# Kernel optimization log

Hardware: AMD Instinct MI355X
Metric: run time of the kernel (lower is better)

Reference implementation:

```python
import jax, jax.numpy as jnp
import numpy as np

E = 1024
H = 16
HD = E // H
FF = 4 * E
B, T = 2, 2048


def _linear_params(key, fan_in, fan_out):
    k1, k2 = jax.random.split(key)
    bound = 1.0 / np.sqrt(fan_in)
    W = jax.random.uniform(k1, (fan_out, fan_in), jnp.float32, -bound, bound)
    b = jax.random.uniform(k2, (fan_out,), jnp.float32, -bound, bound)
    return W, b


def setup_inputs() -> dict:
    key = jax.random.key(0)
    keys = jax.random.split(key, 8)
    x = jax.random.normal(keys[0], (B, T, E), jnp.float32)
    Wq, bq = _linear_params(keys[1], E, E)
    Wk, bk = _linear_params(keys[2], E, E)
    Wv, bv = _linear_params(keys[3], E, E)
    Wo, bo = _linear_params(keys[4], E, E)
    W1, b1 = _linear_params(keys[5], E, FF)
    W2, b2 = _linear_params(keys[6], FF, E)
    ln1_g = jnp.ones((E,), jnp.float32); ln1_b = jnp.zeros((E,), jnp.float32)
    ln2_g = jnp.ones((E,), jnp.float32); ln2_b = jnp.zeros((E,), jnp.float32)
    return {"x": x, "Wq": Wq, "bq": bq, "Wk": Wk, "bk": bk, "Wv": Wv, "bv": bv,
            "Wo": Wo, "bo": bo, "W1": W1, "b1": b1, "W2": W2, "b2": b2,
            "ln1_g": ln1_g, "ln1_b": ln1_b, "ln2_g": ln2_g, "ln2_b": ln2_b}


def _layernorm(x, g, b, eps=1e-5):
    mu = jnp.mean(x, axis=-1, keepdims=True)
    var = jnp.var(x, axis=-1, keepdims=True)
    return (x - mu) * jax.lax.rsqrt(var + eps) * g + b


def reference(x, Wq, bq, Wk, bk, Wv, bv, Wo, bo, W1, b1, W2, b2,
              ln1_g, ln1_b, ln2_g, ln2_b):
    Bc, Tc, Ec = x.shape
    h = _layernorm(x, ln1_g, ln1_b)
    # projections (torch Linear: y = x @ W.T + b)
    q = (h @ Wq.T + bq).reshape(Bc, Tc, H, HD).transpose(0, 2, 1, 3)  # [B,H,T,hd]
    k = (h @ Wk.T + bk).reshape(Bc, Tc, H, HD).transpose(0, 2, 1, 3)
    v = (h @ Wv.T + bv).reshape(Bc, Tc, H, HD).transpose(0, 2, 1, 3)
    scores = jnp.einsum('bhqd,bhkd->bhqk', q, k) / np.sqrt(HD).astype(np.float32)
    causal = jnp.tril(jnp.ones((Tc, Tc), bool))
    scores = jnp.where(causal, scores, -jnp.inf)
    att = jax.nn.softmax(scores, axis=-1)  # dropout = identity (eval)
    out = jnp.einsum('bhqk,bhkd->bhqd', att, v)
    out = out.transpose(0, 2, 1, 3).reshape(Bc, Tc, Ec)
    x = x + out @ Wo.T + bo
    h2 = _layernorm(x, ln2_g, ln2_b)
    ff = jax.nn.relu(h2 @ W1.T + b1) @ W2.T + b2
    return x + ff
```

## Files before the change

### kernel.cpp

```cpp
#include <hip/hip_runtime.h>

typedef unsigned short u16;
typedef __bf16 bf16x8 __attribute__((ext_vector_type(8)));
typedef float f32x4 __attribute__((ext_vector_type(4)));

#define E_ 1024
#define T_ 2048
#define B_ 2
#define H_ 16
#define FF_ 4096
#define M_ 4096

__device__ __forceinline__ u16 f2b(float f) {
    union { float f; unsigned u; } c; c.f = f;
    unsigned r = c.u + 0x7FFFu + ((c.u >> 16) & 1u);
    return (u16)(r >> 16);
}
__device__ __forceinline__ u16 f2bt(float f) {
    union { float f; unsigned u; } c; c.f = f;
    return (u16)(c.u >> 16);
}

__device__ __forceinline__ void gl16(const u16* g, u16* l) {
    __builtin_amdgcn_global_load_lds(
        (__attribute__((address_space(1))) void*)g,
        (__attribute__((address_space(3))) void*)l, 16, 0, 0);
}

__global__ __launch_bounds__(256) void cvt_ln(
        const float* __restrict__ Wq, const float* __restrict__ Wk,
        const float* __restrict__ Wv, const float* __restrict__ Wo,
        const float* __restrict__ W1, const float* __restrict__ W2,
        const float* __restrict__ bq, const float* __restrict__ bk,
        const float* __restrict__ bv,
        u16* __restrict__ WqkvB, u16* __restrict__ WoB,
        u16* __restrict__ W1B, u16* __restrict__ W2B,
        float* __restrict__ bqkv,
        const float* __restrict__ x, const float* __restrict__ g1,
        const float* __restrict__ b1v, u16* __restrict__ hB) {
    if (blockIdx.x < 1024) {
        int row = blockIdx.x * 4 + (threadIdx.x >> 6);
        int t = threadIdx.x & 63;
        const float* xr = x + (size_t)row * E_;
        float v[16];
        float sum = 0.f, ss = 0.f;
#pragma unroll
        for (int c = 0; c < 4; c++) {
            float4 f = *(const float4*)&xr[c * 256 + t * 4];
            v[c * 4 + 0] = f.x; v[c * 4 + 1] = f.y; v[c * 4 + 2] = f.z; v[c * 4 + 3] = f.w;
            sum += f.x + f.y + f.z + f.w;
            ss += f.x * f.x + f.y * f.y + f.z * f.z + f.w * f.w;
        }
#pragma unroll
        for (int d = 32; d; d >>= 1) {
            sum += __shfl_xor(sum, d);
            ss  += __shfl_xor(ss, d);
        }
        float mu = sum * (1.f / E_);
        float var = ss * (1.f / E_) - mu * mu;
        float rs = rsqrtf(var + 1e-5f);
#pragma unroll
        for (int c = 0; c < 4; c++) {
            int idx = c * 256 + t * 4;
            float4 g4 = *(const float4*)&g1[idx];
            float4 b4 = *(const float4*)&b1v[idx];
            ushort4 o;
            o.x = f2b((v[c * 4 + 0] - mu) * rs * g4.x + b4.x);
            o.y = f2b((v[c * 4 + 1] - mu) * rs * g4.y + b4.y);
            o.z = f2b((v[c * 4 + 2] - mu) * rs * g4.z + b4.z);
            o.w = f2b((v[c * 4 + 3] - mu) * rs * g4.w + b4.w);
            *(ushort4*)&hB[(size_t)row * E_ + idx] = o;
        }
        return;
    }
    int i = (blockIdx.x - 1024) * 256 + threadIdx.x;
    if (i >= 3146496) return;
    if (i >= 3145728) {
        int j = i - 3145728;
        const float* s = (j < 256) ? bq : (j < 512) ? bk : bv;
        int jj = j & 255;
        *(float4*)&bqkv[j * 4] = *(const float4*)&s[jj * 4];
        return;
    }
    const float* src; u16* dst; int j;
    if (i < 786432) {
        src = (i < 262144) ? Wq : (i < 524288) ? Wk : Wv;
        j = i & 262143;
        dst = WqkvB + (i >> 18) * (E_ * E_);
    } else if (i < 1048576) { j = i - 786432;  src = Wo; dst = WoB; }
    else if (i < 2097152)   { j = i - 1048576; src = W1; dst = W1B; }
    else                    { j = i - 2097152; src = W2; dst = W2B; }
    float4 f = *(const float4*)&src[j * 4];
    ushort4 o;
    o.x = f2b(f.x); o.y = f2b(f.y); o.z = f2b(f.z); o.w = f2b(f.w);
    *(ushort4*)&dst[j * 4] = o;
}

__global__ __launch_bounds__(64) void ln_fwd(u16* __restrict__ out, const float* __restrict__ x,
                                             const float* __restrict__ g, const float* __restrict__ bta) {
    int row = blockIdx.x;
    int t = threadIdx.x;
    const float* xr = x + (size_t)row * E_;
    float v[16];
    float sum = 0.f, ss = 0.f;
#pragma unroll
    for (int c = 0; c < 4; c++) {
        float4 f = *(const float4*)&xr[c * 256 + t * 4];
        v[c * 4 + 0] = f.x; v[c * 4 + 1] = f.y; v[c * 4 + 2] = f.z; v[c * 4 + 3] = f.w;
        sum += f.x + f.y + f.z + f.w;
        ss += f.x * f.x + f.y * f.y + f.z * f.z + f.w * f.w;
    }
#pragma unroll
    for (int d = 32; d; d >>= 1) {
        sum += __shfl_xor(sum, d);
        ss  += __shfl_xor(ss, d);
    }
    float mu = sum * (1.f / E_);
    float var = ss * (1.f / E_) - mu * mu;
    float rs = rsqrtf(var + 1e-5f);
#pragma unroll
    for (int c = 0; c < 4; c++) {
        int idx = c * 256 + t * 4;
        float4 g4 = *(const float4*)&g[idx];
        float4 b4 = *(const float4*)&bta[idx];
        ushort4 o;
        o.x = f2b((v[c * 4 + 0] - mu) * rs * g4.x + b4.x);
        o.y = f2b((v[c * 4 + 1] - mu) * rs * g4.y + b4.y);
        o.z = f2b((v[c * 4 + 2] - mu) * rs * g4.z + b4.z);
        o.w = f2b((v[c * 4 + 3] - mu) * rs * g4.w + b4.w);
        *(ushort4*)&out[(size_t)row * E_ + idx] = o;
    }
}

template<int BM>
__global__ __launch_bounds__(256) void gemm_bt(
        const u16* __restrict__ A, const u16* __restrict__ Bt,
        const float* __restrict__ bias, const float* __restrict__ residual,
        float* __restrict__ outF, u16* __restrict__ outB, u16* __restrict__ outVt,
        int M, int N, int K, int relu, int qkvmode) {
    constexpr int MT = BM / 32;
    __shared__ __align__(16) u16 As[2][BM * 32];
    __shared__ __align__(16) u16 Bs[2][128 * 32];
    int tid = threadIdx.x;
    int m0 = blockIdx.y * BM, n0 = blockIdx.x * 128;
    int wave = tid >> 6, lane = tid & 63;
    int wm = wave & 1, wn = wave >> 1;
    int r16 = lane & 15, kg = lane >> 4;

    const u16* gA = A + (size_t)(m0 + wave * (BM / 4) + (lane >> 2)) * K + (lane & 3) * 8;
    const u16* gB = Bt + (size_t)(n0 + wave * 32 + (lane >> 2)) * K + (lane & 3) * 8;
    size_t row16 = (size_t)16 * K;
    int aoff = wave * (BM / 4) * 32;
    int boff = wave * 1024;

    f32x4 acc[MT][4] = {};

    const int nk = K >> 5;
    gl16(gA, As[0] + aoff);
    if (BM == 128) gl16(gA + row16, As[0] + aoff + 512);
    gl16(gB, Bs[0] + boff);
    gl16(gB + row16, Bs[0] + boff + 512);

    for (int ks = 0; ks < nk; ks++) {
        int cur = ks & 1;
        __syncthreads();
        if (ks + 1 < nk) {
            int k1 = (ks + 1) << 5;
            int nxt = cur ^ 1;
            gl16(gA + k1, As[nxt] + aoff);
            if (BM == 128) gl16(gA + k1 + row16, As[nxt] + aoff + 512);
            gl16(gB + k1, Bs[nxt] + boff);
            gl16(gB + k1 + row16, Bs[nxt] + boff + 512);
        }

        bf16x8 af[MT], bfr[4];
#pragma unroll
        for (int mt = 0; mt < MT; mt++)
            af[mt] = *(const bf16x8*)&As[cur][(wm * (BM / 2) + mt * 16 + r16) * 32 + kg * 8];
#pragma unroll
        for (int nt = 0; nt < 4; nt++)
            bfr[nt] = *(const bf16x8*)&Bs[cur][(wn * 64 + nt * 16 + r16) * 32 + kg * 8];
#pragma unroll
        for (int mt = 0; mt < MT; mt++)
#pragma unroll
            for (int nt = 0; nt < 4; nt++)
                acc[mt][nt] = __builtin_amdgcn_mfma_f32_16x16x32_bf16(af[mt], bfr[nt], acc[mt][nt], 0, 0, 0);
    }

#pragma unroll
    for (int mt = 0; mt < MT; mt++) {
#pragma unroll
        for (int nt = 0; nt < 4; nt++) {
            int gm = m0 + wm * (BM / 2) + mt * 16 + kg * 4;
            int gn = n0 + wn * 64 + nt * 16 + r16;
            float bv = bias[gn];
            if (qkvmode) {
                if (gn < 2048) {
                    float scl = (gn < 1024) ? 0.18033688f : 1.0f;
#pragma unroll
                    for (int r = 0; r < 4; r++)
                        outB[(size_t)(gm + r) * 2048 + gn] = f2b((acc[mt][nt][r] + bv) * scl);
                } else {
                    int bq_ = gm >> 11, tq = gm & 2047, d = gn - 2048;
                    ushort4 ov;
                    ov.x = f2b(acc[mt][nt][0] + bv);
                    ov.y = f2b(acc[mt][nt][1] + bv);
                    ov.z = f2b(acc[mt][nt][2] + bv);
                    ov.w = f2b(acc[mt][nt][3] + bv);
                    *(ushort4*)&outVt[((size_t)(bq_ * 1024 + d)) * 2048 + tq] = ov;
                }
            } else {
#pragma unroll
                for (int r = 0; r < 4; r++) {
                    float v = acc[mt][nt][r] + bv;
                    size_t off = (size_t)(gm + r) * N + gn;
                    if (residual) v += residual[off];
                    if (relu) v = fmaxf(v, 0.f);
                    if (outF) outF[off] = v;
                    else outB[off] = f2b(v);
                }
            }
        }
    }
}

#define AST 68
__global__ __launch_bounds__(256) void attn_mfma(
        const u16* __restrict__ qk, const u16* __restrict__ vt,
        u16* __restrict__ out) {
    __shared__ __align__(16) u16 Ks[2][64 * AST];
    __shared__ __align__(16) u16 Vs[2][64 * AST];
    __shared__ __align__(16) u16 Ps[4][16 * AST];

    int bz = blockIdx.x;
    int h  = bz & 15;
    int b  = (bz >> 4) & 1;
    int qt = bz >> 5;

    int tid = threadIdx.x;
    int w = tid >> 6, lane = tid & 63;
    int g = lane >> 4, l16 = lane & 15;

    int qrow = qt * 64 + w * 16 + l16;
    bf16x8 qf[2];
    qf[0] = *(const bf16x8*)&qk[(size_t)(b * T_ + qrow) * 2048 + h * 64 + g * 8];
    qf[1] = *(const bf16x8*)&qk[(size_t)(b * T_ + qrow) * 2048 + h * 64 + 32 + g * 8];

    f32x4 o[4] = {};
    f32x4 lp = {0.f, 0.f, 0.f, 0.f};

    int r1 = tid >> 3, col1 = (tid & 7) * 8;
    const u16* gK = qk + (size_t)(b * T_) * 2048 + 1024 + h * 64;
    const u16* gV = vt + (size_t)(b * 1024 + h * 64) * 2048;

    uint4 kr1 = *(const uint4*)&gK[(size_t)r1 * 2048 + col1];
    uint4 kr2 = *(const uint4*)&gK[(size_t)(r1 + 32) * 2048 + col1];
    uint4 vr1 = *(const uint4*)&gV[(size_t)r1 * 2048 + col1];
    uint4 vr2 = *(const uint4*)&gV[(size_t)(r1 + 32) * 2048 + col1];

    for (int t = 0; t <= qt; t++) {
        int cur = t & 1;
        *(uint4*)&Ks[cur][r1 * AST + col1] = kr1;
        *(uint4*)&Ks[cur][(r1 + 32) * AST + col1] = kr2;
        *(uint4*)&Vs[cur][r1 * AST + col1] = vr1;
        *(uint4*)&Vs[cur][(r1 + 32) * AST + col1] = vr2;
        __syncthreads();
        if (t < qt) {
            int j1 = (t + 1) * 64;
            kr1 = *(const uint4*)&gK[(size_t)(j1 + r1) * 2048 + col1];
            kr2 = *(const uint4*)&gK[(size_t)(j1 + r1 + 32) * 2048 + col1];
            vr1 = *(const uint4*)&gV[(size_t)r1 * 2048 + j1 + col1];
            vr2 = *(const uint4*)&gV[(size_t)(r1 + 32) * 2048 + j1 + col1];
        }

        f32x4 s[4];
#pragma unroll
        for (int nt = 0; nt < 4; nt++) {
            f32x4 c16 = {-16.f, -16.f, -16.f, -16.f};
            bf16x8 k0 = *(const bf16x8*)&Ks[cur][(nt * 16 + l16) * AST + g * 8];
            bf16x8 k1 = *(const bf16x8*)&Ks[cur][(nt * 16 + l16) * AST + 32 + g * 8];
            s[nt] = __builtin_amdgcn_mfma_f32_16x16x32_bf16(qf[0], k0, c16, 0, 0, 0);
            s[nt] = __builtin_amdgcn_mfma_f32_16x16x32_bf16(qf[1], k1, s[nt], 0, 0, 0);
        }

        if (t == qt) {
            int j0 = t * 64;
#pragma unroll
            for (int nt = 0; nt < 4; nt++) {
                int key = j0 + nt * 16 + l16;
#pragma unroll
                for (int r = 0; r < 4; r++) {
                    int q = qt * 64 + w * 16 + g * 4 + r;
                    if (key > q) s[nt][r] = -INFINITY;
                }
            }
        }

#pragma unroll
        for (int nt = 0; nt < 4; nt++)
#pragma unroll
            for (int r = 0; r < 4; r++) {
                float p = exp2f(s[nt][r]);
                lp[r] += p;
                Ps[w][(g * 4 + r) * AST + nt * 16 + l16] = f2bt(p);
            }

#pragma unroll
        for (int kf = 0; kf < 2; kf++) {
            bf16x8 pf = *(const bf16x8*)&Ps[w][l16 * AST + kf * 32 + g * 8];
#pragma unroll
            for (int nt = 0; nt < 4; nt++) {
                bf16x8 vf = *(const bf16x8*)&Vs[cur][(nt * 16 + l16) * AST + kf * 32 + g * 8];
                o[nt] = __builtin_amdgcn_mfma_f32_16x16x32_bf16(pf, vf, o[nt], 0, 0, 0);
            }
        }
    }

#pragma unroll
    for (int x = 1; x <= 8; x <<= 1)
#pragma unroll
        for (int r = 0; r < 4; r++)
            lp[r] += __shfl_xor(lp[r], x);

    float inv[4];
#pragma unroll
    for (int r = 0; r < 4; r++) inv[r] = 1.f / lp[r];
    int qg = qt * 64 + w * 16 + g * 4;
#pragma unroll
    for (int nt = 0; nt < 4; nt++)
#pragma unroll
        for (int r = 0; r < 4; r++)
            out[(size_t)(b * T_ + qg + r) * E_ + h * 64 + nt * 16 + l16] =
                f2b(o[nt][r] * inv[r]);
}

extern "C" void kernel_launch(void* const* d_in, const int* in_sizes, int n_in,
                              void* d_out, int out_size, void* d_ws, size_t ws_size,
                              hipStream_t stream) {
    const float* x    = (const float*)d_in[0];
    const float* Wq   = (const float*)d_in[1];
    const float* bq   = (const float*)d_in[2];
    const float* Wk   = (const float*)d_in[3];
    const float* bk   = (const float*)d_in[4];
    const float* Wv   = (const float*)d_in[5];
    const float* bv   = (const float*)d_in[6];
    const float* Wo   = (const float*)d_in[7];
    const float* bo   = (const float*)d_in[8];
    const float* W1   = (const float*)d_in[9];
    const float* b1   = (const float*)d_in[10];
    const float* W2   = (const float*)d_in[11];
    const float* b2   = (const float*)d_in[12];
    const float* ln1g = (const float*)d_in[13];
    const float* ln1b = (const float*)d_in[14];
    const float* ln2g = (const float*)d_in[15];
    const float* ln2b = (const float*)d_in[16];

    char* ws = (char*)d_ws;
    size_t off = 0;
    auto alloc = [&](size_t bytes) { char* p = ws + off; off += (bytes + 255) & ~(size_t)255; return p; };

    u16*   hB    = (u16*)  alloc((size_t)M_ * E_ * 2);
    u16*   WqkvB = (u16*)  alloc((size_t)3 * E_ * E_ * 2);
    u16*   WoB   = (u16*)  alloc((size_t)E_ * E_ * 2);
    u16*   W1B   = (u16*)  alloc((size_t)FF_ * E_ * 2);
    u16*   W2B   = (u16*)  alloc((size_t)E_ * FF_ * 2);
    float* bqkv  = (float*)alloc(3 * E_ * 4);
    u16*   qkB   = (u16*)  alloc((size_t)M_ * 2 * E_ * 2);
    u16*   vtG   = (u16*)  alloc((size_t)M_ * E_ * 2);
    u16*   attnB = (u16*)  alloc((size_t)M_ * E_ * 2);
    float* x2    = (float*)alloc((size_t)M_ * E_ * 4);
    u16*   h2B   = (u16*)  alloc((size_t)M_ * E_ * 2);
    u16*   rB    = (u16*)  alloc((size_t)M_ * FF_ * 2);

    cvt_ln<<<1024 + 12291, 256, 0, stream>>>(Wq, Wk, Wv, Wo, W1, W2, bq, bk, bv,
                                             WqkvB, WoB, W1B, W2B, bqkv,
                                             x, ln1g, ln1b, hB);

    gemm_bt<128><<<dim3(3 * E_ / 128, M_ / 128), 256, 0, stream>>>(
        hB, WqkvB, bqkv, nullptr, nullptr, qkB, vtG, M_, 3 * E_, E_, 0, 1);

    attn_mfma<<<B_ * H_ * (T_ / 64), 256, 0, stream>>>(qkB, vtG, attnB);

    gemm_bt<64><<<dim3(E_ / 128, M_ / 64), 256, 0, stream>>>(
        attnB, WoB, bo, x, x2, nullptr, nullptr, M_, E_, E_, 0, 0);

    ln_fwd<<<M_, 64, 0, stream>>>(h2B, x2, ln2g, ln2b);

    gemm_bt<128><<<dim3(FF_ / 128, M_ / 128), 256, 0, stream>>>(
        h2B, W1B, b1, nullptr, nullptr, rB, nullptr, M_, FF_, E_, 1, 0);

    gemm_bt<64><<<dim3(E_ / 128, M_ / 64), 256, 0, stream>>>(
        rB, W2B, b2, x2, (float*)d_out, nullptr, nullptr, M_, E_, FF_, 0, 0);
}
```

Baseline: 392.0 us.

## Triple-buffer GEMM LDS tiles with explicit vmcnt waits; larger tile for FFN down-proj

The GEMM main loop moves from double to triple buffering. It prefetches two k-steps ahead and uses s_waitcnt vmcnt with a single barrier per iteration instead of a full drain before each step, so global-to-LDS loads overlap more with the MFMA work. The W2 down-projection also switches from 64-row to 128-row tiles, which halves its grid to 256 blocks. The changes use more LDS per block and cut parallelism for that GEMM, and correctness depends on the vmcnt counts matching the number of loads issued.

```diff
diff --git a/kernel.cpp b/kernel.cpp
--- a/kernel.cpp
+++ b/kernel.cpp
@@ -139,8 +139,8 @@
         float* __restrict__ outF, u16* __restrict__ outB, u16* __restrict__ outVt,
         int M, int N, int K, int relu, int qkvmode) {
     constexpr int MT = BM / 32;
-    __shared__ __align__(16) u16 As[2][BM * 32];
-    __shared__ __align__(16) u16 Bs[2][128 * 32];
+    __shared__ __align__(16) u16 As[3][BM * 32];
+    __shared__ __align__(16) u16 Bs[3][128 * 32];
     int tid = threadIdx.x;
     int m0 = blockIdx.y * BM, n0 = blockIdx.x * 128;
     int wave = tid >> 6, lane = tid & 63;
@@ -156,36 +156,50 @@
     f32x4 acc[MT][4] = {};
 
     const int nk = K >> 5;
-    gl16(gA, As[0] + aoff);
-    if (BM == 128) gl16(gA + row16, As[0] + aoff + 512);
-    gl16(gB, Bs[0] + boff);
-    gl16(gB + row16, Bs[0] + boff + 512);
-
-    for (int ks = 0; ks < nk; ks++) {
-        int cur = ks & 1;
-        __syncthreads();
-        if (ks + 1 < nk) {
-            int k1 = (ks + 1) << 5;
-            int nxt = cur ^ 1;
-            gl16(gA + k1, As[nxt] + aoff);
-            if (BM == 128) gl16(gA + k1 + row16, As[nxt] + aoff + 512);
-            gl16(gB + k1, Bs[nxt] + boff);
-            gl16(gB + k1 + row16, Bs[nxt] + boff + 512);
-        }
-
+
+    auto issue = [&](int kt, int buf) {
+        int k1 = kt << 5;
+        gl16(gA + k1, As[buf] + aoff);
+        if (BM == 128) gl16(gA + k1 + row16, As[buf] + aoff + 512);
+        gl16(gB + k1, Bs[buf] + boff);
+        gl16(gB + k1 + row16, Bs[buf] + boff + 512);
+    };
+
+    auto compute = [&](int cb) {
         bf16x8 af[MT], bfr[4];
 #pragma unroll
         for (int mt = 0; mt < MT; mt++)
-            af[mt] = *(const bf16x8*)&As[cur][(wm * (BM / 2) + mt * 16 + r16) * 32 + kg * 8];
+            af[mt] = *(const bf16x8*)&As[cb][(wm * (BM / 2) + mt * 16 + r16) * 32 + kg * 8];
 #pragma unroll
         for (int nt = 0; nt < 4; nt++)
-            bfr[nt] = *(const bf16x8*)&Bs[cur][(wn * 64 + nt * 16 + r16) * 32 + kg * 8];
+            bfr[nt] = *(const bf16x8*)&Bs[cb][(wn * 64 + nt * 16 + r16) * 32 + kg * 8];
 #pragma unroll
         for (int mt = 0; mt < MT; mt++)
 #pragma unroll
             for (int nt = 0; nt < 4; nt++)
                 acc[mt][nt] = __builtin_amdgcn_mfma_f32_16x16x32_bf16(af[mt], bfr[nt], acc[mt][nt], 0, 0, 0);
-    }
+    };
+
+    issue(0, 0);
+    issue(1, 1);
+
+    int cur = 0;
+    for (int ks = 0; ks < nk - 1; ks++) {
+        if (BM == 128) asm volatile("s_waitcnt vmcnt(4)" ::: "memory");
+        else           asm volatile("s_waitcnt vmcnt(3)" ::: "memory");
+        __builtin_amdgcn_s_barrier();
+        asm volatile("" ::: "memory");
+        if (ks + 2 < nk) {
+            int p2 = cur ? cur - 1 : 2;
+            issue(ks + 2, p2);
+        }
+        compute(cur);
+        cur = (cur < 2) ? cur + 1 : 0;
+    }
+    asm volatile("s_waitcnt vmcnt(0)" ::: "memory");
+    __builtin_amdgcn_s_barrier();
+    asm volatile("" ::: "memory");
+    compute(cur);
 
 #pragma unroll
     for (int mt = 0; mt < MT; mt++) {
@@ -389,6 +403,6 @@
     gemm_bt<128><<<dim3(FF_ / 128, M_ / 128), 256, 0, stream>>>(
         h2B, W1B, b1, nullptr, nullptr, rB, nullptr, M_, FF_, E_, 1, 0);
 
-    gemm_bt<64><<<dim3(E_ / 128, M_ / 64), 256, 0, stream>>>(
+    gemm_bt<128><<<dim3(E_ / 128, M_ / 128), 256, 0, stream>>>(
         rB, W2B, b2, x2, (float*)d_out, nullptr, nullptr, M_, E_, FF_, 0, 0);
 }
```

Result: slower. 409.2 us (+4.4%).
